# Kernel optimization log

Hardware: AMD Instinct MI355X
Metric: run time of the kernel (lower is better)

Reference implementation:

```python
import jax, jax.numpy as jnp
import numpy as np

DIM = 1024
B, TI, TJ = 8, 2048, 2048
EPS = 1e-5


def layernorm(x, g, b):
    mu = jnp.mean(x, axis=-1, keepdims=True)
    var = jnp.var(x, axis=-1, keepdims=True)
    return (x - mu) * jax.lax.rsqrt(var + EPS) * g + b


def setup_inputs() -> dict:
    key = jax.random.key(0)
    ks = jax.random.split(key, 12)
    s = 1.0 / np.sqrt(DIM)
    return {
        "target": jax.random.normal(ks[0], (B, TI, DIM), jnp.float32),
        "source_k": jax.random.normal(ks[1], (B, TJ, DIM), jnp.float32),
        "source_v": jax.random.normal(ks[2], (B, TJ, DIM), jnp.float32),
        "Wq": jax.random.uniform(ks[3], (DIM, DIM), jnp.float32, -s, s),
        "bq": jax.random.uniform(ks[4], (DIM,), jnp.float32, -s, s),
        "Wk": jax.random.uniform(ks[5], (DIM, DIM), jnp.float32, -s, s),
        "bk": jax.random.uniform(ks[6], (DIM,), jnp.float32, -s, s),
        "Wv": jax.random.uniform(ks[7], (DIM, DIM), jnp.float32, -s, s),
        "bv": jax.random.uniform(ks[8], (DIM,), jnp.float32, -s, s),
        "g_t": jnp.ones((DIM,), jnp.float32),
        "b_t": jnp.zeros((DIM,), jnp.float32),
        "g_k": jnp.ones((DIM,), jnp.float32),
        "b_k": jnp.zeros((DIM,), jnp.float32),
        "g_v": jnp.ones((DIM,), jnp.float32),
        "b_v": jnp.zeros((DIM,), jnp.float32),
    }


def reference(target, source_k, source_v, Wq, bq, Wk, bk, Wv, bv,
              g_t, b_t, g_k, b_k, g_v, b_v):
    scale = DIM ** (-0.5)
    t = layernorm(target, g_t, b_t)
    sk = layernorm(source_k, g_k, b_k)
    sv = layernorm(source_v, g_v, b_v)
    # torch Linear: x @ W.T + b
    q = jnp.einsum('bid,ed->bie', t, Wq) + bq
    k = jnp.einsum('bjd,ed->bje', sk, Wk) + bk
    v = jnp.einsum('bjd,ed->bje', sv, Wv) + bv
    dots = jnp.einsum('bid,bjd->bij', q, k) * scale
    attn = jax.nn.softmax(dots, axis=2)
    return jnp.einsum('bij,bjd->bid', attn, v)
```

## Files before the change

### kernel.cpp

```cpp
#include <hip/hip_runtime.h>
#include <cstdint>

using u16 = unsigned short;
using u32 = unsigned int;
typedef __attribute__((ext_vector_type(8))) short short8;
typedef __attribute__((ext_vector_type(4))) float f32x4;

__device__ __forceinline__ float bf2f(u16 u) { return __uint_as_float(((u32)u) << 16); }
__device__ __forceinline__ u16 f2bf(float f) {
    u32 u = __float_as_uint(f);
    u32 r = u + 0x7fffu + ((u >> 16) & 1u);
    return (u16)(r >> 16);
}

__device__ __forceinline__ void load_lds16(const void* g, void* l) {
    __builtin_amdgcn_global_load_lds((const __attribute__((address_space(1))) void*)g,
                                     (__attribute__((address_space(3))) void*)l, 16, 0, 0);
}

__device__ __forceinline__ void ln_row(const float* __restrict__ x,
                                       const float* __restrict__ gw,
                                       const float* __restrict__ bw,
                                       u16* __restrict__ y, int row) {
    const int tid = threadIdx.x;
    const float4 v = ((const float4*)(x + (size_t)row * 1024))[tid];
    float s  = v.x + v.y + v.z + v.w;
    float ss = v.x * v.x + v.y * v.y + v.z * v.z + v.w * v.w;
#pragma unroll
    for (int off = 32; off; off >>= 1) {
        s  += __shfl_xor(s, off);
        ss += __shfl_xor(ss, off);
    }
    __shared__ float sm[8];
    const int lane = tid & 63, wid = tid >> 6;
    if (lane == 0) { sm[wid] = s; sm[wid + 4] = ss; }
    __syncthreads();
    s  = sm[0] + sm[1] + sm[2] + sm[3];
    ss = sm[4] + sm[5] + sm[6] + sm[7];
    const float mu   = s * (1.0f / 1024.0f);
    const float var  = ss * (1.0f / 1024.0f) - mu * mu;
    const float rstd = rsqrtf(var + 1e-5f);
    const float4 g4 = ((const float4*)gw)[tid];
    const float4 b4 = ((const float4*)bw)[tid];
    u16 o[4];
    o[0] = f2bf((v.x - mu) * rstd * g4.x + b4.x);
    o[1] = f2bf((v.y - mu) * rstd * g4.y + b4.y);
    o[2] = f2bf((v.z - mu) * rstd * g4.z + b4.z);
    o[3] = f2bf((v.w - mu) * rstd * g4.w + b4.w);
    *(uint2*)(y + (size_t)row * 1024 + tid * 4) = *(uint2*)o;
}

__global__ __launch_bounds__(256)
void ln_cast_kernel(const float* __restrict__ x, const float* __restrict__ gw,
                    const float* __restrict__ bw, u16* __restrict__ y) {
    ln_row(x, gw, bw, y, blockIdx.x);
}

__global__ __launch_bounds__(256)
void ln3_kernel(const float* __restrict__ x0, const float* __restrict__ x1,
                const float* __restrict__ x2,
                const float* __restrict__ g0, const float* __restrict__ g1,
                const float* __restrict__ g2,
                const float* __restrict__ b0, const float* __restrict__ b1,
                const float* __restrict__ b2, u16* __restrict__ y) {
    const int bid = blockIdx.x;
    const int sel = bid >> 14;
    const int row = bid & 16383;
    const float* x  = (sel == 0) ? x0 : (sel == 1) ? x1 : x2;
    const float* gw = (sel == 0) ? g0 : (sel == 1) ? g1 : g2;
    const float* bw = (sel == 0) ? b0 : (sel == 1) ? b1 : b2;
    ln_row(x, gw, bw, y + ((size_t)sel << 24), row);
}

__global__ __launch_bounds__(256)
void cast3_kernel(const float* __restrict__ wa, const float* __restrict__ wb,
                  const float* __restrict__ wc, u16* __restrict__ oa) {
    const int bid = blockIdx.x;
    const int sel = bid >> 10;
    const float* s = (sel == 0) ? wa : (sel == 1) ? wb : wc;
    u16* d = oa + (size_t)sel * 1048576;
    const int i = (bid & 1023) * 256 + threadIdx.x;
    const float4 v = ((const float4*)s)[i];
    u16 o[4] = { f2bf(v.x), f2bf(v.y), f2bf(v.z), f2bf(v.w) };
    *(uint2*)(d + (size_t)i * 4) = *(uint2*)o;
}

template<int MODE>
__global__ __launch_bounds__(256, (MODE == 3 ? 3 : 4))
void gemm_bt(const u16* __restrict__ A, const u16* __restrict__ B,
             const float* __restrict__ bias0, const float* __restrict__ bias1,
             const float* __restrict__ bias2,
             void* __restrict__ Cout, void* __restrict__ Cout2,
             const int M, const int N, const int K, const float scale,
             const long sA, const long sB, const long sC)
{
    int bz, m0, n0;
    if (MODE == 2 || MODE == 3) {
        const int id = blockIdx.x;
        bz = id & 7;
        m0 = ((id >> 3) & 15) * 128;
        n0 = (id >> 7) * 128;
    } else {
        bz = (MODE == 4) ? blockIdx.z : 0;
        m0 = blockIdx.x * 128;
        n0 = blockIdx.y * 128;
    }
    A += (long)bz * sA;
    B += (long)bz * sB;
    const float* bias = (MODE == 4) ? (bz == 0 ? bias0 : bz == 1 ? bias1 : bias2)
                                    : bias0;
    __shared__ __align__(16) u16 As[128 * 64];
    __shared__ __align__(16) u16 Bs[128 * 64];
    const int tid  = threadIdx.x;
    const int lane = tid & 63, wid = tid >> 6;
    const int wm = (wid & 1) * 64, wn = (wid >> 1) * 64;

    const int scol = (tid & 7) ^ ((tid >> 3) & 7);
    const u16* ap = A + (long)(m0 + (tid >> 3)) * K + scol * 8;
    const u16* bp = B + (long)(n0 + (tid >> 3)) * K + scol * 8;
    u16* asd = As + wid * 512;
    u16* bsd = Bs + wid * 512;
    const long rs32 = 32L * K;

    f32x4 acc[4][4] = {};
    f32x4 acc_l[4] = {};
    const short8 ones8 = {16256, 16256, 16256, 16256, 16256, 16256, 16256, 16256};
    const int fr = lane & 15, fq = lane >> 4;
    const int sw = (fq ^ (fr & 7)) * 8;
    const int offA0 = (wm + fr) * 64 + sw;
    const int offA1 = offA0 ^ 32;
    const int offB0 = (wn + fr) * 64 + sw;
    const int offB1 = offB0 ^ 32;

    for (int k0 = 0; k0 < K; k0 += 64) {
#pragma unroll
        for (int rd = 0; rd < 4; rd++) {
            load_lds16(ap + k0 + rd * rs32, asd + rd * 2048);
            load_lds16(bp + k0 + rd * rs32, bsd + rd * 2048);
        }
        __syncthreads();
#pragma unroll
        for (int s = 0; s < 2; s++) {
            const int oa = s ? offA1 : offA0;
            const int ob = s ? offB1 : offB0;
            short8 b0 = *(const short8*)&Bs[ob];
            short8 b1 = *(const short8*)&Bs[ob + 1024];
            short8 b2 = *(const short8*)&Bs[ob + 2048];
            short8 b3 = *(const short8*)&Bs[ob + 3072];
#pragma unroll
            for (int i = 0; i < 4; i++) {
                const short8 a = *(const short8*)&As[oa + i * 1024];
                acc[i][0] = __builtin_amdgcn_mfma_f32_16x16x32_bf16(a, b0, acc[i][0], 0, 0, 0);
                acc[i][1] = __builtin_amdgcn_mfma_f32_16x16x32_bf16(a, b1, acc[i][1], 0, 0, 0);
                acc[i][2] = __builtin_amdgcn_mfma_f32_16x16x32_bf16(a, b2, acc[i][2], 0, 0, 0);
                acc[i][3] = __builtin_amdgcn_mfma_f32_16x16x32_bf16(a, b3, acc[i][3], 0, 0, 0);
                if (MODE == 3)
                    acc_l[i] = __builtin_amdgcn_mfma_f32_16x16x32_bf16(a, ones8, acc_l[i], 0, 0, 0);
            }
        }
        __syncthreads();
    }

    const int cn = lane & 15;
    const int cm = (lane >> 4) * 4;
    float invl[4][4];
    if (MODE == 3) {
#pragma unroll
        for (int i = 0; i < 4; i++)
#pragma unroll
            for (int r = 0; r < 4; r++) invl[i][r] = 1.0f / acc_l[i][r];
    }
#pragma unroll
    for (int i = 0; i < 4; i++) {
        const int gmb = m0 + wm + i * 16 + cm;
#pragma unroll
        for (int j = 0; j < 4; j++) {
            const int gn = n0 + wn + j * 16 + cn;
            const float bv = (MODE <= 1 || MODE == 4) ? bias[gn] : 0.0f;
            if (MODE == 1 || (MODE == 4 && bz == 2)) {
                u16* dst = (MODE == 4) ? (u16*)Cout2 : (u16*)Cout;
                const int batch = gmb >> 11;
                const int jj = gmb & 2047;
                u16 o[4];
#pragma unroll
                for (int r = 0; r < 4; r++) o[r] = f2bf(acc[i][j][r] + bv);
                *(uint2*)(dst + ((long)batch * N + gn) * 2048 + jj) = *(uint2*)o;
            } else if (MODE == 0 || MODE == 4) {
                u16* dst = (u16*)Cout + ((MODE == 4) ? (long)bz * 16777216 : 0);
#pragma unroll
                for (int r = 0; r < 4; r++)
                    dst[(long)(gmb + r) * N + gn] = f2bf(acc[i][j][r] + bv);
            } else {
#pragma unroll
                for (int r = 0; r < 4; r++) {
                    const long gm = gmb + r;
                    float v = acc[i][j][r];
                    if (MODE == 2) v = __expf(v * scale);
                    if (MODE == 3)
                        ((float*)Cout)[(long)bz * sC + gm * N + gn] = v * invl[i][r];
                    else
                        ((u16*)Cout)[(long)bz * sC + gm * N + gn] = f2bf(v);
                }
            }
        }
    }
}

__device__ __forceinline__ void ph_mid() {
    __builtin_amdgcn_sched_barrier(0);
    __builtin_amdgcn_s_barrier();
    asm volatile("s_waitcnt lgkmcnt(0)" ::: "memory");
    __builtin_amdgcn_sched_barrier(0);
}
__device__ __forceinline__ void ph_end() {
    __builtin_amdgcn_sched_barrier(0);
    __builtin_amdgcn_s_barrier();
    __builtin_amdgcn_sched_barrier(0);
}

#define RDAH(reg, mh) do { \
    aF[0] = *(const short8*)&(reg)[ offA + ((mh)*4+0)*1024];        \
    aF[1] = *(const short8*)&(reg)[(offA + ((mh)*4+0)*1024) ^ 32];  \
    aF[2] = *(const short8*)&(reg)[ offA + ((mh)*4+1)*1024];        \
    aF[3] = *(const short8*)&(reg)[(offA + ((mh)*4+1)*1024) ^ 32];  \
    aF[4] = *(const short8*)&(reg)[ offA + ((mh)*4+2)*1024];        \
    aF[5] = *(const short8*)&(reg)[(offA + ((mh)*4+2)*1024) ^ 32];  \
    aF[6] = *(const short8*)&(reg)[ offA + ((mh)*4+3)*1024];        \
    aF[7] = *(const short8*)&(reg)[(offA + ((mh)*4+3)*1024) ^ 32];  } while (0)

#define RDBH(dst, reg, nh) do { \
    dst[0] = *(const short8*)&(reg)[ offB + ((nh)*2+0)*1024];        \
    dst[1] = *(const short8*)&(reg)[(offB + ((nh)*2+0)*1024) ^ 32];  \
    dst[2] = *(const short8*)&(reg)[ offB + ((nh)*2+1)*1024];        \
    dst[3] = *(const short8*)&(reg)[(offB + ((nh)*2+1)*1024) ^ 32];  } while (0)

#define MMQ(mh, nh, bF) do { \
    __builtin_amdgcn_s_setprio(1); \
    _Pragma("unroll") \
    for (int i_ = 0; i_ < 4; i_++) { \
        _Pragma("unroll") \
        for (int j_ = 0; j_ < 2; j_++) { \
            acc[(mh)*4+i_][(nh)*2+j_] = __builtin_amdgcn_mfma_f32_16x16x32_bf16( \
                aF[2*i_],   bF[2*j_],   acc[(mh)*4+i_][(nh)*2+j_], 0, 0, 0); \
            acc[(mh)*4+i_][(nh)*2+j_] = __builtin_amdgcn_mfma_f32_16x16x32_bf16( \
                aF[2*i_+1], bF[2*j_+1], acc[(mh)*4+i_][(nh)*2+j_], 0, 0, 0); \
        } \
    } \
    __builtin_amdgcn_s_setprio(0); } while (0)

#define STA(reg, hm, kt) do { \
    const u16* s_ = apg + (hm) * rH + (long)(kt) * 64; \
    u16* d_ = (reg) + (hm) * 8192 + w * 1024; \
    load_lds16(s_, d_); \
    load_lds16(s_ + rK8, d_ + 512); } while (0)

#define STB(reg, hm, kt) do { \
    const u16* s_ = bpg + (hm) * rH + (long)(kt) * 64; \
    u16* d_ = (reg) + (hm) * 8192 + w * 1024; \
    load_lds16(s_, d_); \
    load_lds16(s_ + rK8, d_ + 512); } while (0)

template<int MODE>
__global__ __launch_bounds__(512, 1)
void gemm8(const u16* __restrict__ A, const u16* __restrict__ B,
           const float* __restrict__ bias0, const float* __restrict__ bias1,
           const float* __restrict__ bias2,
           void* __restrict__ Cout, void* __restrict__ Cout2,
           const int M, const int N, const int K, const float scale,
           const long sA, const long sB, const long sC)
{
    int bz, m0, n0;
    if (MODE == 2) {
        const int id = blockIdx.x;
        bz = id & 7;
        m0 = ((id >> 3) & 7) * 256;
        n0 = (id >> 6) * 256;
    } else {
        bz = blockIdx.z;
        m0 = blockIdx.x * 256;
        n0 = blockIdx.y * 256;
    }
    A += (long)bz * sA;
    B += (long)bz * sB;
    const float* bias = (MODE == 4) ? (bz == 0 ? bias0 : bz == 1 ? bias1 : bias2)
                                    : bias0;

    __shared__ __align__(16) u16 lds[65536];
    u16* const Ar0 = lds;
    u16* const Ar1 = lds + 16384;
    u16* const Br0 = lds + 32768;
    u16* const Br1 = lds + 49152;

    const int tid = threadIdx.x;
    const int w = tid >> 6, l = tid & 63;
    const int cgrp = (l & 7) ^ ((l >> 3) & 7);
    const long rK8 = 8L * K;
    const long rH  = 128L * K;
    const u16* apg = A + (long)(m0 + w * 16 + (l >> 3)) * K + cgrp * 8;
    const u16* bpg = B + (long)(n0 + w * 16 + (l >> 3)) * K + cgrp * 8;

    const int wm = (w & 1) * 128;
    const int wn = (w >> 1) * 64;
    const int fr = l & 15, fq = l >> 4;
    const int sw8 = (fq ^ (fr & 7)) * 8;
    const int offA = (wm + fr) * 64 + sw8;
    const int offB = (wn + fr) * 64 + sw8;

    f32x4 acc[8][4] = {};
    short8 aF[8];
    short8 bF0[4], bF1[4];

    STB(Br0, 0, 0); STB(Br0, 1, 0); STA(Ar0, 0, 0); STA(Ar0, 1, 0);
    STB(Br1, 0, 1); STB(Br1, 1, 1); STA(Ar1, 0, 1); STA(Ar1, 1, 1);
    __builtin_amdgcn_sched_barrier(0);
    asm volatile("s_waitcnt vmcnt(8)" ::: "memory");
    __builtin_amdgcn_s_barrier();
    asm volatile("" ::: "memory");
    __builtin_amdgcn_sched_barrier(0);

    const int NI = K >> 7;
    for (int it = 0; it < NI; ++it) {
        const bool nl = (it < NI - 1);
        const int t2 = 2 * it + 2, t3 = 2 * it + 3;
        RDAH(Ar0, 0); RDBH(bF0, Br0, 0);
        ph_mid();
        MMQ(0, 0, bF0);
        ph_end();
        RDBH(bF1, Br0, 1);
        ph_mid();
        MMQ(0, 1, bF1);
        ph_end();
        RDAH(Ar0, 1);
        if (nl) { STB(Br0, 0, t2); STB(Br0, 1, t2); }
        ph_mid();
        MMQ(1, 0, bF0);
        ph_end();
        if (nl) { STA(Ar0, 0, t2); STA(Ar0, 1, t2); }
        ph_mid();
        MMQ(1, 1, bF1);
        __builtin_amdgcn_sched_barrier(0);
        if (nl) asm volatile("s_waitcnt vmcnt(8)" ::: "memory");
        else    asm volatile("s_waitcnt vmcnt(0)" ::: "memory");
        __builtin_amdgcn_s_barrier();
        asm volatile("" ::: "memory");
        __builtin_amdgcn_sched_barrier(0);
        RDAH(Ar1, 0); RDBH(bF0, Br1, 0);
        ph_mid();
        MMQ(0, 0, bF0);
        ph_end();
        RDBH(bF1, Br1, 1);
        ph_mid();
        MMQ(0, 1, bF1);
        ph_end();
        RDAH(Ar1, 1);
        if (nl) { STB(Br1, 0, t3); STB(Br1, 1, t3); }
        ph_mid();
        MMQ(1, 0, bF0);
        ph_end();
        if (nl) { STA(Ar1, 0, t3); STA(Ar1, 1, t3); }
        ph_mid();
        MMQ(1, 1, bF1);
        __builtin_amdgcn_sched_barrier(0);
        if (nl) asm volatile("s_waitcnt vmcnt(8)" ::: "memory");
        else    asm volatile("s_waitcnt vmcnt(0)" ::: "memory");
        __builtin_amdgcn_s_barrier();
        asm volatile("" ::: "memory");
        __builtin_amdgcn_sched_barrier(0);
    }

    const int cn = l & 15, cm = (l >> 4) * 4;
#pragma unroll
    for (int i = 0; i < 8; i++) {
        const int gmb = m0 + wm + i * 16 + cm;
#pragma unroll
        for (int j = 0; j < 4; j++) {
            const int gn = n0 + wn + j * 16 + cn;
            if (MODE == 4) {
                const float bv = bias[gn];
                if (bz == 2) {
                    const int batch = gmb >> 11, jj = gmb & 2047;
                    u16 o[4];
#pragma unroll
                    for (int r = 0; r < 4; r++) o[r] = f2bf(acc[i][j][r] + bv);
                    *(uint2*)((u16*)Cout2 + ((long)batch * N + gn) * 2048 + jj) = *(uint2*)o;
                } else {
                    u16* dst = (u16*)Cout + (long)bz * ((long)M * N);
#pragma unroll
                    for (int r = 0; r < 4; r++)
                        dst[(long)(gmb + r) * N + gn] = f2bf(acc[i][j][r] + bv);
                }
            } else {
#pragma unroll
                for (int r = 0; r < 4; r++)
                    ((u16*)Cout)[(long)bz * sC + (long)(gmb + r) * N + gn] =
                        f2bf(__expf(acc[i][j][r] * scale));
            }
        }
    }
}

extern "C" void kernel_launch(void* const* d_in, const int* in_sizes, int n_in,
                              void* d_out, int out_size, void* d_ws, size_t ws_size,
                              hipStream_t stream) {
    const float* target = (const float*)d_in[0];
    const float* src_k  = (const float*)d_in[1];
    const float* src_v  = (const float*)d_in[2];
    const float* Wq = (const float*)d_in[3];
    const float* bq = (const float*)d_in[4];
    const float* Wk = (const float*)d_in[5];
    const float* bk = (const float*)d_in[6];
    const float* Wv = (const float*)d_in[7];
    const float* bv = (const float*)d_in[8];
    const float* g_t = (const float*)d_in[9];
    const float* b_t = (const float*)d_in[10];
    const float* g_k = (const float*)d_in[11];
    const float* b_k = (const float*)d_in[12];
    const float* g_v = (const float*)d_in[13];
    const float* b_v = (const float*)d_in[14];

    char* ws = (char*)d_ws;
    const float scale = 0.03125f;
    const size_t MB = 1048576;

    if (ws_size >= 198 * MB) {
        u16* q   = (u16*)(ws + 0);
        u16* kk  = (u16*)(ws + 32 * MB);
        u16* vT  = (u16*)(ws + 64 * MB);
        u16* ln3 = (u16*)(ws + 96 * MB);
        u16* wqb = (u16*)(ws + 192 * MB);
        u16* S   = (u16*)(ws + 96 * MB);

        cast3_kernel<<<3072, 256, 0, stream>>>(Wq, Wk, Wv, wqb);
        ln3_kernel<<<49152, 256, 0, stream>>>(target, src_k, src_v,
                                              g_t, g_k, g_v, b_t, b_k, b_v, ln3);
        gemm8<4><<<dim3(64, 4, 3), 512, 0, stream>>>(ln3, wqb, bq, bk, bv,
            q, vT, 16384, 1024, 1024, 1.0f, 16777216L, 1048576L, 0);
        gemm8<2><<<512, 512, 0, stream>>>(q, kk, nullptr, nullptr, nullptr, S, nullptr,
            2048, 2048, 1024, scale, 2048L * 1024, 2048L * 1024, 2048L * 2048);
        gemm_bt<3><<<1024, 256, 0, stream>>>(S, vT, nullptr, nullptr, nullptr, d_out, nullptr,
            2048, 1024, 2048, 1.0f, 2048L * 2048, 1024L * 2048, 2048L * 1024);
    } else {
        u16* q   = (u16*)(ws + 0);
        u16* kk  = (u16*)(ws + 32 * MB);
        u16* vT  = (u16*)(ws + 64 * MB);
        u16* ln  = (u16*)(ws + 96 * MB);
        u16* wqb = (u16*)(ws + 128 * MB);
        u16* wkb = wqb + 1048576;
        u16* wvb = wkb + 1048576;
        u16* S   = (u16*)(ws + 96 * MB);

        cast3_kernel<<<3072, 256, 0, stream>>>(Wq, Wk, Wv, wqb);
        ln_cast_kernel<<<16384, 256, 0, stream>>>(target, g_t, b_t, ln);
        gemm_bt<0><<<dim3(128, 8, 1), 256, 0, stream>>>(ln, wqb, bq, nullptr, nullptr,
            q, nullptr, 16384, 1024, 1024, 1.0f, 0, 0, 0);
        ln_cast_kernel<<<16384, 256, 0, stream>>>(src_k, g_k, b_k, ln);
        gemm_bt<0><<<dim3(128, 8, 1), 256, 0, stream>>>(ln, wkb, bk, nullptr, nullptr,
            kk, nullptr, 16384, 1024, 1024, 1.0f, 0, 0, 0);
        ln_cast_kernel<<<16384, 256, 0, stream>>>(src_v, g_v, b_v, ln);
        gemm_bt<1><<<dim3(128, 8, 1), 256, 0, stream>>>(ln, wvb, bv, nullptr, nullptr,
            vT, nullptr, 16384, 1024, 1024, 1.0f, 0, 0, 0);
        gemm_bt<2><<<2048, 256, 0, stream>>>(q, kk, nullptr, nullptr, nullptr, S, nullptr,
            2048, 2048, 1024, scale, 2048L * 1024, 2048L * 1024, 2048L * 2048);
        gemm_bt<3><<<1024, 256, 0, stream>>>(S, vT, nullptr, nullptr, nullptr, d_out, nullptr,
            2048, 1024, 2048, 1.0f, 2048L * 2048, 1024L * 2048, 2048L * 1024);
    }
}
```

Before: 504.9 us.

## Remap warp tiles across LDS halves and spread global-to-LDS loads across phases

Each warp's 128x64 output tile is re-mapped so it covers a 64-row slice in each of the two 128-row A halves and a 32-column slice in each B half, rather than one contiguous block. Because each phase then reads only one LDS half, the first half of each buffer can be refilled earlier. The global-to-LDS loads are spread more evenly across the four MFMA phases. The MFMA loop is also reordered so that consecutive instructions do not depend on the same accumulator. The epilogue index math is updated to match, at the cost of a less contiguous store pattern.

```diff
diff --git a/kernel.cpp b/kernel.cpp
--- a/kernel.cpp
+++ b/kernel.cpp
@@ -219,31 +219,31 @@
 }
 
 #define RDAH(reg, mh) do { \
-    aF[0] = *(const short8*)&(reg)[ offA + ((mh)*4+0)*1024];        \
-    aF[1] = *(const short8*)&(reg)[(offA + ((mh)*4+0)*1024) ^ 32];  \
-    aF[2] = *(const short8*)&(reg)[ offA + ((mh)*4+1)*1024];        \
-    aF[3] = *(const short8*)&(reg)[(offA + ((mh)*4+1)*1024) ^ 32];  \
-    aF[4] = *(const short8*)&(reg)[ offA + ((mh)*4+2)*1024];        \
-    aF[5] = *(const short8*)&(reg)[(offA + ((mh)*4+2)*1024) ^ 32];  \
-    aF[6] = *(const short8*)&(reg)[ offA + ((mh)*4+3)*1024];        \
-    aF[7] = *(const short8*)&(reg)[(offA + ((mh)*4+3)*1024) ^ 32];  } while (0)
+    aF[0] = *(const short8*)&(reg)[ offA + (mh)*8192 + 0*1024];        \
+    aF[1] = *(const short8*)&(reg)[(offA + (mh)*8192 + 0*1024) ^ 32];  \
+    aF[2] = *(const short8*)&(reg)[ offA + (mh)*8192 + 1*1024];        \
+    aF[3] = *(const short8*)&(reg)[(offA + (mh)*8192 + 1*1024) ^ 32];  \
+    aF[4] = *(const short8*)&(reg)[ offA + (mh)*8192 + 2*1024];        \
+    aF[5] = *(const short8*)&(reg)[(offA + (mh)*8192 + 2*1024) ^ 32];  \
+    aF[6] = *(const short8*)&(reg)[ offA + (mh)*8192 + 3*1024];        \
+    aF[7] = *(const short8*)&(reg)[(offA + (mh)*8192 + 3*1024) ^ 32];  } while (0)
 
 #define RDBH(dst, reg, nh) do { \
-    dst[0] = *(const short8*)&(reg)[ offB + ((nh)*2+0)*1024];        \
-    dst[1] = *(const short8*)&(reg)[(offB + ((nh)*2+0)*1024) ^ 32];  \
-    dst[2] = *(const short8*)&(reg)[ offB + ((nh)*2+1)*1024];        \
-    dst[3] = *(const short8*)&(reg)[(offB + ((nh)*2+1)*1024) ^ 32];  } while (0)
+    dst[0] = *(const short8*)&(reg)[ offB + (nh)*8192 + 0*1024];        \
+    dst[1] = *(const short8*)&(reg)[(offB + (nh)*8192 + 0*1024) ^ 32];  \
+    dst[2] = *(const short8*)&(reg)[ offB + (nh)*8192 + 1*1024];        \
+    dst[3] = *(const short8*)&(reg)[(offB + (nh)*8192 + 1*1024) ^ 32];  } while (0)
 
 #define MMQ(mh, nh, bF) do { \
     __builtin_amdgcn_s_setprio(1); \
     _Pragma("unroll") \
-    for (int i_ = 0; i_ < 4; i_++) { \
+    for (int s_ = 0; s_ < 2; s_++) { \
         _Pragma("unroll") \
-        for (int j_ = 0; j_ < 2; j_++) { \
-            acc[(mh)*4+i_][(nh)*2+j_] = __builtin_amdgcn_mfma_f32_16x16x32_bf16( \
-                aF[2*i_],   bF[2*j_],   acc[(mh)*4+i_][(nh)*2+j_], 0, 0, 0); \
-            acc[(mh)*4+i_][(nh)*2+j_] = __builtin_amdgcn_mfma_f32_16x16x32_bf16( \
-                aF[2*i_+1], bF[2*j_+1], acc[(mh)*4+i_][(nh)*2+j_], 0, 0, 0); \
+        for (int i_ = 0; i_ < 4; i_++) { \
+            _Pragma("unroll") \
+            for (int j_ = 0; j_ < 2; j_++) \
+                acc[(mh)*4+i_][(nh)*2+j_] = __builtin_amdgcn_mfma_f32_16x16x32_bf16( \
+                    aF[2*i_+s_], bF[2*j_+s_], acc[(mh)*4+i_][(nh)*2+j_], 0, 0, 0); \
         } \
     } \
     __builtin_amdgcn_s_setprio(0); } while (0)
@@ -299,12 +299,12 @@
     const u16* apg = A + (long)(m0 + w * 16 + (l >> 3)) * K + cgrp * 8;
     const u16* bpg = B + (long)(n0 + w * 16 + (l >> 3)) * K + cgrp * 8;
 
-    const int wm = (w & 1) * 128;
-    const int wn = (w >> 1) * 64;
+    const int w1 = w & 1;
+    const int wn2 = (w >> 1) * 32;
     const int fr = l & 15, fq = l >> 4;
     const int sw8 = (fq ^ (fr & 7)) * 8;
-    const int offA = (wm + fr) * 64 + sw8;
-    const int offB = (wn + fr) * 64 + sw8;
+    const int offA = (w1 * 64 + fr) * 64 + sw8;
+    const int offB = (wn2 + fr) * 64 + sw8;
 
     f32x4 acc[8][4] = {};
     short8 aF[8];
@@ -327,15 +327,16 @@
         MMQ(0, 0, bF0);
         ph_end();
         RDBH(bF1, Br0, 1);
+        if (nl) { STB(Br0, 0, t2); STA(Ar0, 0, t2); }
         ph_mid();
         MMQ(0, 1, bF1);
         ph_end();
         RDAH(Ar0, 1);
-        if (nl) { STB(Br0, 0, t2); STB(Br0, 1, t2); }
+        if (nl) STB(Br0, 1, t2);
         ph_mid();
         MMQ(1, 0, bF0);
         ph_end();
-        if (nl) { STA(Ar0, 0, t2); STA(Ar0, 1, t2); }
+        if (nl) STA(Ar0, 1, t2);
         ph_mid();
         MMQ(1, 1, bF1);
         __builtin_amdgcn_sched_barrier(0);
@@ -349,15 +350,16 @@
         MMQ(0, 0, bF0);
         ph_end();
         RDBH(bF1, Br1, 1);
+        if (nl) { STB(Br1, 0, t3); STA(Ar1, 0, t3); }
         ph_mid();
         MMQ(0, 1, bF1);
         ph_end();
         RDAH(Ar1, 1);
-        if (nl) { STB(Br1, 0, t3); STB(Br1, 1, t3); }
+        if (nl) STB(Br1, 1, t3);
         ph_mid();
         MMQ(1, 0, bF0);
         ph_end();
-        if (nl) { STA(Ar1, 0, t3); STA(Ar1, 1, t3); }
+        if (nl) STA(Ar1, 1, t3);
         ph_mid();
         MMQ(1, 1, bF1);
         __builtin_amdgcn_sched_barrier(0);
@@ -371,10 +373,10 @@
     const int cn = l & 15, cm = (l >> 4) * 4;
 #pragma unroll
     for (int i = 0; i < 8; i++) {
-        const int gmb = m0 + wm + i * 16 + cm;
+        const int gmb = m0 + (i >> 2) * 128 + w1 * 64 + (i & 3) * 16 + cm;
 #pragma unroll
         for (int j = 0; j < 4; j++) {
-            const int gn = n0 + wn + j * 16 + cn;
+            const int gn = n0 + (j >> 1) * 128 + wn2 + (j & 1) * 16 + cn;
             if (MODE == 4) {
                 const float bv = bias[gn];
                 if (bz == 2) {
```

New measurement: 496.1 us. Within noise of the previous version (-1.7%).
